# Kernel tuning notes

Measured on AMD Instinct MI355X. Metric: run time of the kernel, lower is better.

## Reference

```python
import jax, jax.numpy as jnp
import numpy as np

N_NODES = 100000
N_EDGES = 1600000
D = 64            # embedding_dim
D2 = D * D        # GRUCell hidden/input size


def gru_cell(x, h, w_ih, w_hh, b_ih, b_hh):
    # PyTorch GRUCell math. x, h: [D2]; w_ih, w_hh: [3*D2, D2]; b_*: [3*D2]
    gi = w_ih @ x + b_ih
    gh = w_hh @ h + b_hh
    i_r, i_z, i_n = jnp.split(gi, 3)
    h_r, h_z, h_n = jnp.split(gh, 3)
    r = jax.nn.sigmoid(i_r + h_r)
    z = jax.nn.sigmoid(i_z + h_z)
    n = jnp.tanh(i_n + r * h_n)
    return (1.0 - z) * n + z * h


def gcn_layer(x, w, src, dst, edge_norm):
    # dense transform then degree-normalized gather-scatter aggregation
    h = x @ w                                   # [N, D]
    m = h[src] * edge_norm[:, None]             # [E, D] messages
    return jax.ops.segment_sum(m, dst, num_segments=N_NODES)


def setup_inputs() -> dict:
    key = jax.random.key(0)
    ks = jax.random.split(key, 12)
    s = 0.02  # keep GRU gates in a sane range
    return {
        "node_embeddings": jax.random.normal(ks[0], (N_NODES, D), jnp.float32),
        "gc1_weights": jax.random.normal(ks[1], (D, D), jnp.float32) * s,
        "gc2_weights": jax.random.normal(ks[2], (D, D), jnp.float32) * s,
        "gc1_hist": jax.random.normal(ks[3], (D, D), jnp.float32) * s,
        "gc2_hist": jax.random.normal(ks[4], (D, D), jnp.float32) * s,
        "w_ih": jax.random.normal(ks[5], (3 * D2, D2), jnp.float32) * s,
        "w_hh": jax.random.normal(ks[6], (3 * D2, D2), jnp.float32) * s,
        "b_ih": jax.random.normal(ks[7], (3 * D2,), jnp.float32) * s,
        "b_hh": jax.random.normal(ks[8], (3 * D2,), jnp.float32) * s,
        "src": jax.random.randint(ks[9], (N_EDGES,), 0, N_NODES, jnp.int32),
        "dst": jax.random.randint(ks[10], (N_EDGES,), 0, N_NODES, jnp.int32),
    }


def reference(node_embeddings, gc1_weights, gc2_weights, gc1_hist, gc2_hist,
              w_ih, w_hh, b_ih, b_hh, src, dst):
    # --- weight evolution (GRUCell over flattened GCN weights) ---
    w1 = gru_cell(gc1_hist.reshape(-1), gc1_weights.reshape(-1),
                  w_ih, w_hh, b_ih, b_hh).reshape(D, D)
    w2 = gru_cell(gc2_hist.reshape(-1), gc2_weights.reshape(-1),
                  w_ih, w_hh, b_ih, b_hh).reshape(D, D)

    # --- symmetric degree normalization (in-degree, clamped at 1) ---
    deg = jax.ops.segment_sum(jnp.ones_like(dst, jnp.float32), dst,
                              num_segments=N_NODES)
    norm = jnp.clip(deg, 1.0, None) ** -0.5     # [N]
    edge_norm = norm[src] * norm[dst]           # [E]

    # --- two GCN layers ---
    x = jax.nn.relu(gcn_layer(node_embeddings, w1, src, dst, edge_norm))
    x = gcn_layer(x, w2, src, dst, edge_norm)
    return x
```

## Files before the change

kernel.cpp:

```cpp
#include <hip/hip_runtime.h>

typedef unsigned int uint_t;
typedef float v4f __attribute__((ext_vector_type(4)));

#define N_NODES 100000
#define N_EDGES 1600000
#define D 64
#define D2 4096
#define D3 12288

#define NPAD 100352u

#define BSHIFT 9
#define BNODES 512
#define NBUCK 196
#define CHUNK 8192
#define CAP   16384
#define GRUBLK 3072
#define XBLK  ((N_NODES + 255) / 256)

#define OFF_GI1   0u
#define OFF_GI2   (OFF_GI1 + D3)
#define OFF_GH1   (OFF_GI2 + D3)
#define OFF_GH2   (OFF_GH1 + D3)
#define OFF_W1    (OFF_GH2 + D3)
#define OFF_W2    (OFF_W1 + D2)
#define OFF_DEG   (OFF_W2 + D2)
#define OFF_BCUR  (OFF_DEG + NPAD)
#define OFF_ROWS  (OFF_BCUR + 256u)
#define OFF_CSR   (OFF_ROWS + NPAD)
#define OFF_XP    (OFF_CSR + 1600000u)
#define OFF_Y1    (OFF_XP + 3200000u)
#define OFF_PAIRS (OFF_Y1 + 3200000u)

__device__ __forceinline__ float dot4v(v4f a, float4 b, float acc) {
    acc = fmaf(a[0], b.x, acc);
    acc = fmaf(a[1], b.y, acc);
    acc = fmaf(a[2], b.z, acc);
    acc = fmaf(a[3], b.w, acc);
    return acc;
}

__device__ __forceinline__ uint_t bfr(float f) {
    uint_t u = __float_as_uint(f);
    u += 0x7FFFu + ((u >> 16) & 1u);
    return u >> 16;
}

struct PartLds {
    int hist[256];
    int lbase[256];
    int gbase[256];
    int lcur[256];
    int2 stage[CHUNK];
};
struct GruLds {
    float4 sA[1024];
    float4 sB[1024];
};

__global__ __launch_bounds__(512) void mega1(
    const float* __restrict__ w_ih, const float* __restrict__ w_hh,
    const float* __restrict__ x1, const float* __restrict__ x2,
    const float* __restrict__ h1, const float* __restrict__ h2,
    float* __restrict__ gi1, float* __restrict__ gi2,
    float* __restrict__ gh1, float* __restrict__ gh2,
    const int* __restrict__ src, const int* __restrict__ dst,
    int* __restrict__ deg, int* __restrict__ bcur, int2* __restrict__ pairs)
{
    __shared__ __align__(16) char ldsraw[sizeof(PartLds)];
    const int tid = threadIdx.x;

    if (blockIdx.x < NBUCK) {
        PartLds& P = *reinterpret_cast<PartLds*>(ldsraw);
        const int e0  = blockIdx.x * CHUNK;
        const int cnt = min(CHUNK, N_EDGES - e0);

        if (tid < 256) { P.hist[tid] = 0; P.lcur[tid] = 0; }
        __syncthreads();
        for (int i = tid; i < cnt; i += 512) {
            const int d = dst[e0 + i];
            atomicAdd(&deg[d], 1);
            atomicAdd(&P.hist[d >> BSHIFT], 1);
        }
        __syncthreads();
        if (tid < 256) P.lbase[tid] = P.hist[tid];
        __syncthreads();
        for (int off = 1; off < 256; off <<= 1) {
            int a = 0, b = 0;
            if (tid < 256) { a = P.lbase[tid]; b = (tid >= off) ? P.lbase[tid - off] : 0; }
            __syncthreads();
            if (tid < 256) P.lbase[tid] = a + b;
            __syncthreads();
        }
        if (tid < 256) {
            const int c = P.hist[tid];
            P.lbase[tid] -= c;
            P.gbase[tid] = c ? atomicAdd(&bcur[tid], c) : 0;
        }
        __syncthreads();
        for (int i = tid; i < cnt; i += 512) {
            const int s = src[e0 + i], d = dst[e0 + i];
            const int b = d >> BSHIFT;
            const int p = P.lbase[b] + atomicAdd(&P.lcur[b], 1);
            P.stage[p] = make_int2(s, d);
        }
        __syncthreads();
        for (int i = tid; i < cnt; i += 512) {
            const int2 v = P.stage[i];
            const int b = v.y >> BSHIFT;
            const int gp = P.gbase[b] + (i - P.lbase[b]);
            if (gp < CAP) pairs[(size_t)b * CAP + gp] = v;
        }
    } else {
        GruLds& G = *reinterpret_cast<GruLds*>(ldsraw);
        const int gb   = blockIdx.x - NBUCK;
        const int half = (gb >= GRUBLK / 2);
        const int blk  = gb - (half ? GRUBLK / 2 : 0);

        {
            const float4* va = (const float4*)(half ? h1 : x1);
            const float4* vb = (const float4*)(half ? h2 : x2);
#pragma unroll
            for (int i = 0; i < 2; ++i) {
                const int k = tid + i * 512;
                G.sA[k] = va[k];
                G.sB[k] = vb[k];
            }
        }
        __syncthreads();

        const int wave = tid >> 6, lane = tid & 63;
        const int row  = blk * 8 + wave;
        const v4f* wr = (const v4f*)((half ? w_hh : w_ih) + (size_t)row * D2);

        float p0 = 0.f, p1 = 0.f;
#pragma unroll
        for (int g = 0; g < 4; ++g) {
            v4f a[4];
#pragma unroll
            for (int k = 0; k < 4; ++k)
                a[k] = __builtin_nontemporal_load(&wr[lane + (g * 4 + k) * 64]);
#pragma unroll
            for (int k = 0; k < 4; ++k) {
                const int idx = lane + (g * 4 + k) * 64;
                p0 = dot4v(a[k], G.sA[idx], p0);
                p1 = dot4v(a[k], G.sB[idx], p1);
            }
        }
#pragma unroll
        for (int m = 32; m > 0; m >>= 1) {
            p0 += __shfl_down(p0, m, 64);
            p1 += __shfl_down(p1, m, 64);
        }
        if (lane == 0) {
            float* oA = half ? gh1 : gi1;
            float* oB = half ? gh2 : gi2;
            oA[row] = p0;
            oB[row] = p1;
        }
    }
}

struct CsrLds {
    int lofs[BNODES];
    int lcur[BNODES];
    int pscan[256];
    int bscan[256];
    int stage[CAP];
};

__global__ __launch_bounds__(256) void mega2(
    const int2* __restrict__ pairs, const int* __restrict__ deg,
    const int* __restrict__ bcnt, int* __restrict__ rowstart,
    int* __restrict__ csr_src,
    const float* __restrict__ emb,
    const float* __restrict__ gi1, const float* __restrict__ gh1,
    const float* __restrict__ gi2, const float* __restrict__ gh2,
    const float* __restrict__ b_ih, const float* __restrict__ b_hh,
    const float* __restrict__ hw1, const float* __restrict__ hw2,
    float* __restrict__ w1, float* __restrict__ w2,
    unsigned short* __restrict__ xp)
{
    __shared__ __align__(16) char ldsraw[sizeof(CsrLds)];
    const int tid = threadIdx.x;

    if (blockIdx.x < NBUCK) {
        CsrLds& L = *reinterpret_cast<CsrLds*>(ldsraw);
        const int b = blockIdx.x;
        const int nodeBase = b << BSHIFT;

        const int cb = (tid < NBUCK) ? bcnt[tid] : 0;
        L.bscan[tid] = cb;
        __syncthreads();
        for (int off = 1; off < 256; off <<= 1) {
            int a = L.bscan[tid];
            int x = (tid >= off) ? L.bscan[tid - off] : 0;
            __syncthreads();
            L.bscan[tid] = a + x;
            __syncthreads();
        }
        const int cnt  = bcnt[b];
        const int base = L.bscan[b] - cnt;

        const int n0 = nodeBase + 2 * tid;
        const int d0 = (n0     < N_NODES) ? deg[n0]     : 0;
        const int d1 = (n0 + 1 < N_NODES) ? deg[n0 + 1] : 0;
        L.pscan[tid] = d0 + d1;
        __syncthreads();
        for (int off = 1; off < 256; off <<= 1) {
            int a = L.pscan[tid];
            int x = (tid >= off) ? L.pscan[tid - off] : 0;
            __syncthreads();
            L.pscan[tid] = a + x;
            __syncthreads();
        }
        const int ex = L.pscan[tid] - (d0 + d1);
        L.lofs[2 * tid]     = ex;
        L.lofs[2 * tid + 1] = ex + d0;
        L.lcur[2 * tid]     = 0;
        L.lcur[2 * tid + 1] = 0;

        if (n0     < N_NODES) rowstart[n0]     = base + ex;
        if (n0 + 1 < N_NODES) rowstart[n0 + 1] = base + ex + d0;
        __syncthreads();

        const int2* bp = pairs + (size_t)b * CAP;
        for (int i = tid; i < cnt; i += 256) {
            const int2 v = bp[i];
            const int ln = v.y - nodeBase;
            const int p  = L.lofs[ln] + atomicAdd(&L.lcur[ln], 1);
            L.stage[p] = v.x;
        }
        __syncthreads();
        for (int i = tid; i < cnt; i += 256)
            csr_src[base + i] = L.stage[i];
    } else if (blockIdx.x < NBUCK + 2) {
        const int layer = blockIdx.x - NBUCK;
        const float* gi = layer ? gi2 : gi1;
        const float* gh = layer ? gh2 : gh1;
        const float* hw = layer ? hw2 : hw1;
        float* wo = layer ? w2 : w1;
#pragma unroll
        for (int i = 0; i < 16; ++i) {
            const int j = tid + i * 256;
            float ir = gi[j]          + b_ih[j];
            float hr = gh[j]          + b_hh[j];
            float iz = gi[j + D2]     + b_ih[j + D2];
            float hz = gh[j + D2]     + b_hh[j + D2];
            float in_ = gi[j + 2*D2]  + b_ih[j + 2*D2];
            float hn = gh[j + 2*D2]   + b_hh[j + 2*D2];
            float r = 1.f / (1.f + expf(-(ir + hr)));
            float z = 1.f / (1.f + expf(-(iz + hz)));
            float n = tanhf(in_ + r * hn);
            wo[j] = (1.f - z) * n + z * hw[j];
        }
    } else {
        const int node = (blockIdx.x - NBUCK - 2) * 256 + tid;
        if (node >= N_NODES) return;
        const float nn = rsqrtf(fmaxf((float)deg[node], 1.0f));
        const float4* p = (const float4*)(emb + (size_t)node * D);
        uint_t pk[32];
#pragma unroll
        for (int i = 0; i < 16; ++i) {
            float4 u = p[i];
            pk[2*i]   = bfr(u.x * nn) | (bfr(u.y * nn) << 16);
            pk[2*i+1] = bfr(u.z * nn) | (bfr(u.w * nn) << 16);
        }
        uint4* po = (uint4*)(xp + (size_t)node * D);
#pragma unroll
        for (int i = 0; i < 8; ++i)
            po[i] = make_uint4(pk[4*i], pk[4*i+1], pk[4*i+2], pk[4*i+3]);
    }
}

template <bool LAYER1>
__global__ __launch_bounds__(256) void gcn_layer_kernel(
    const unsigned short* __restrict__ xbf, const float* __restrict__ w,
    const int* __restrict__ csr_src, const int* __restrict__ rowstart,
    const int* __restrict__ degv, void* __restrict__ out)
{
    __shared__ float sw[D2];
    __shared__ float xr[4][8][68];
    const int tid = threadIdx.x;
#pragma unroll
    for (int i = 0; i < 16; ++i) sw[tid + i * 256] = w[tid + i * 256];
    __syncthreads();

    const int node = blockIdx.x * 32 + (tid >> 3);
    const int lg   = tid & 7;
    const int wv   = tid >> 6;
    const int slot = (tid >> 3) & 7;
    const uint4* hp = (const uint4*)xbf;
    const bool active = (node < N_NODES);
    int dg = 0;

    if (active) {
        const int beg = rowstart[node];
        dg = degv[node];

        float acc[8];
#pragma unroll
        for (int c = 0; c < 8; ++c) acc[c] = 0.f;

        int k = 0;
        for (; k + 8 <= dg; k += 8) {
            int s[8];
#pragma unroll
            for (int u = 0; u < 8; ++u) s[u] = csr_src[beg + k + u];
            uint4 r[8];
#pragma unroll
            for (int u = 0; u < 8; ++u) r[u] = hp[(size_t)s[u] * 8 + lg];
#pragma unroll
            for (int u = 0; u < 8; ++u) {
                acc[0] += __uint_as_float(r[u].x << 16);
                acc[1] += __uint_as_float(r[u].x & 0xFFFF0000u);
                acc[2] += __uint_as_float(r[u].y << 16);
                acc[3] += __uint_as_float(r[u].y & 0xFFFF0000u);
                acc[4] += __uint_as_float(r[u].z << 16);
                acc[5] += __uint_as_float(r[u].z & 0xFFFF0000u);
                acc[6] += __uint_as_float(r[u].w << 16);
                acc[7] += __uint_as_float(r[u].w & 0xFFFF0000u);
            }
        }
        for (; k < dg; ++k) {
            const int s = csr_src[beg + k];
            const uint4 r = hp[(size_t)s * 8 + lg];
            acc[0] += __uint_as_float(r.x << 16);
            acc[1] += __uint_as_float(r.x & 0xFFFF0000u);
            acc[2] += __uint_as_float(r.y << 16);
            acc[3] += __uint_as_float(r.y & 0xFFFF0000u);
            acc[4] += __uint_as_float(r.z << 16);
            acc[5] += __uint_as_float(r.z & 0xFFFF0000u);
            acc[6] += __uint_as_float(r.w << 16);
            acc[7] += __uint_as_float(r.w & 0xFFFF0000u);
        }

        const float nn = rsqrtf(fmaxf((float)dg, 1.0f));
#pragma unroll
        for (int c = 0; c < 8; ++c) xr[wv][slot][lg * 8 + c] = acc[c] * nn;
    }
    __syncthreads();

    if (active) {
        float o[8];
#pragma unroll
        for (int c = 0; c < 8; ++c) o[c] = 0.f;
#pragma unroll
        for (int k = 0; k < D; ++k) {
            const float xv = xr[wv][slot][k];
#pragma unroll
            for (int c = 0; c < 8; ++c)
                o[c] = fmaf(xv, sw[k * D + lg * 8 + c], o[c]);
        }
        if (LAYER1) {
            const float nn = rsqrtf(fmaxf((float)dg, 1.0f));
            float t[8];
#pragma unroll
            for (int c = 0; c < 8; ++c) t[c] = fmaxf(o[c], 0.f) * nn;
            uint4 pk;
            pk.x = bfr(t[0]) | (bfr(t[1]) << 16);
            pk.y = bfr(t[2]) | (bfr(t[3]) << 16);
            pk.z = bfr(t[4]) | (bfr(t[5]) << 16);
            pk.w = bfr(t[6]) | (bfr(t[7]) << 16);
            ((uint4*)out)[(size_t)node * 8 + lg] = pk;
        } else {
            float* op = (float*)out + (size_t)node * D + (size_t)lg * 8;
            *(float4*)(op)     = make_float4(o[0], o[1], o[2], o[3]);
            *(float4*)(op + 4) = make_float4(o[4], o[5], o[6], o[7]);
        }
    }
}

extern "C" void kernel_launch(void* const* d_in, const int* in_sizes, int n_in,
                              void* d_out, int out_size, void* d_ws, size_t ws_size,
                              hipStream_t stream)
{
    const float* emb  = (const float*)d_in[0];
    const float* gc1w = (const float*)d_in[1];
    const float* gc2w = (const float*)d_in[2];
    const float* gc1h = (const float*)d_in[3];
    const float* gc2h = (const float*)d_in[4];
    const float* w_ih = (const float*)d_in[5];
    const float* w_hh = (const float*)d_in[6];
    const float* b_ih = (const float*)d_in[7];
    const float* b_hh = (const float*)d_in[8];
    const int* src = (const int*)d_in[9];
    const int* dst = (const int*)d_in[10];

    float* ws = (float*)d_ws;
    float* gi1 = ws + OFF_GI1;
    float* gi2 = ws + OFF_GI2;
    float* gh1 = ws + OFF_GH1;
    float* gh2 = ws + OFF_GH2;
    float* w1  = ws + OFF_W1;
    float* w2  = ws + OFF_W2;
    int*   deg = (int*)(ws + OFF_DEG);
    int*   bcur = (int*)(ws + OFF_BCUR);
    int*   rows = (int*)(ws + OFF_ROWS);
    int*   csr  = (int*)(ws + OFF_CSR);
    unsigned short* xp = (unsigned short*)(ws + OFF_XP);
    unsigned short* y1 = (unsigned short*)(ws + OFF_Y1);
    int2*  pairs = (int2*)(ws + OFF_PAIRS);
    float* out  = (float*)d_out;

    hipMemsetAsync(deg, 0, (NPAD + 256) * sizeof(int), stream);

    mega1<<<NBUCK + GRUBLK, 512, 0, stream>>>(
        w_ih, w_hh, gc1h, gc2h, gc1w, gc2w, gi1, gi2, gh1, gh2,
        src, dst, deg, bcur, pairs);

    mega2<<<NBUCK + 2 + XBLK, 256, 0, stream>>>(
        pairs, deg, bcur, rows, csr, emb,
        gi1, gh1, gi2, gh2, b_ih, b_hh, gc1w, gc2w, w1, w2, xp);

    gcn_layer_kernel<true><<<(N_NODES + 31) / 32, 256, 0, stream>>>(
        xp, w1, csr, rows, deg, y1);

    gcn_layer_kernel<false><<<(N_NODES + 31) / 32, 256, 0, stream>>>(
        y1, w2, csr, rows, deg, out);
}
```

Before: 569.5 us.

## Split bf16 features into column slices and separate gather from dense transform

Node features are now stored as four 16-column bf16 slices, each its own contiguous array. The gather is a separate kernel that runs one pass per slice, so each pass's random-access working set (about 3.2 MB) is more likely to stay in cache. The dense 64x64 transform moves to its own kernel with one thread per node and 64 accumulators in registers. This adds a round trip through an fp32 intermediate buffer and extra launches, and risks heavy register pressure in the transform kernel.

```diff
diff --git a/kernel.cpp b/kernel.cpp
--- a/kernel.cpp
+++ b/kernel.cpp
@@ -18,6 +18,9 @@
 #define CAP   16384
 #define GRUBLK 3072
 #define XBLK  ((N_NODES + 255) / 256)
+
+#define SLICE_US 1600000u
+#define GCHUNKS  ((N_NODES + 127) / 128)
 
 #define OFF_GI1   0u
 #define OFF_GI2   (OFF_GI1 + D3)
@@ -32,6 +35,7 @@
 #define OFF_XP    (OFF_CSR + 1600000u)
 #define OFF_Y1    (OFF_XP + 3200000u)
 #define OFF_PAIRS (OFF_Y1 + 3200000u)
+#define OFF_G     OFF_PAIRS
 
 __device__ __forceinline__ float dot4v(v4f a, float4 b, float acc) {
     acc = fmaf(a[0], b.x, acc);
@@ -45,6 +49,21 @@
     uint_t u = __float_as_uint(f);
     u += 0x7FFFu + ((u >> 16) & 1u);
     return u >> 16;
+}
+
+__device__ __forceinline__ void store_sliced(
+    unsigned short* base, int node, const float* t)
+{
+#pragma unroll
+    for (int p = 0; p < 4; ++p) {
+        uint_t pk[8];
+#pragma unroll
+        for (int j = 0; j < 8; ++j)
+            pk[j] = bfr(t[p*16 + 2*j]) | (bfr(t[p*16 + 2*j + 1]) << 16);
+        uint4* po = (uint4*)(base + (size_t)p * SLICE_US + (size_t)node * 16);
+        po[0] = make_uint4(pk[0], pk[1], pk[2], pk[3]);
+        po[1] = make_uint4(pk[4], pk[5], pk[6], pk[7]);
+    }
 }
 
 struct PartLds {
@@ -260,115 +279,119 @@
         if (node >= N_NODES) return;
         const float nn = rsqrtf(fmaxf((float)deg[node], 1.0f));
         const float4* p = (const float4*)(emb + (size_t)node * D);
-        uint_t pk[32];
+        float t[D];
 #pragma unroll
         for (int i = 0; i < 16; ++i) {
             float4 u = p[i];
-            pk[2*i]   = bfr(u.x * nn) | (bfr(u.y * nn) << 16);
-            pk[2*i+1] = bfr(u.z * nn) | (bfr(u.w * nn) << 16);
-        }
-        uint4* po = (uint4*)(xp + (size_t)node * D);
-#pragma unroll
-        for (int i = 0; i < 8; ++i)
-            po[i] = make_uint4(pk[4*i], pk[4*i+1], pk[4*i+2], pk[4*i+3]);
-    }
+            t[4*i+0] = u.x * nn; t[4*i+1] = u.y * nn;
+            t[4*i+2] = u.z * nn; t[4*i+3] = u.w * nn;
+        }
+        store_sliced(xp, node, t);
+    }
+}
+
+__global__ __launch_bounds__(256) void gather_slice_kernel(
+    const unsigned short* __restrict__ xs, const int* __restrict__ csr_src,
+    const int* __restrict__ rowstart, const int* __restrict__ degv,
+    float* __restrict__ g)
+{
+    const int tid   = threadIdx.x;
+    const int pass  = blockIdx.x & 3;
+    const int chunk = blockIdx.x >> 2;
+    const int node  = chunk * 128 + (tid >> 1);
+    if (node >= N_NODES) return;
+    const int half = tid & 1;
+    const uint4* sp = (const uint4*)(xs + (size_t)pass * SLICE_US);
+
+    const int beg = rowstart[node];
+    const int dg  = degv[node];
+
+    float acc[8];
+#pragma unroll
+    for (int c = 0; c < 8; ++c) acc[c] = 0.f;
+
+    int k = 0;
+    for (; k + 8 <= dg; k += 8) {
+        int s[8];
+#pragma unroll
+        for (int u = 0; u < 8; ++u) s[u] = csr_src[beg + k + u];
+        uint4 r[8];
+#pragma unroll
+        for (int u = 0; u < 8; ++u) r[u] = sp[(size_t)s[u] * 2 + half];
+#pragma unroll
+        for (int u = 0; u < 8; ++u) {
+            acc[0] += __uint_as_float(r[u].x << 16);
+            acc[1] += __uint_as_float(r[u].x & 0xFFFF0000u);
+            acc[2] += __uint_as_float(r[u].y << 16);
+            acc[3] += __uint_as_float(r[u].y & 0xFFFF0000u);
+            acc[4] += __uint_as_float(r[u].z << 16);
+            acc[5] += __uint_as_float(r[u].z & 0xFFFF0000u);
+            acc[6] += __uint_as_float(r[u].w << 16);
+            acc[7] += __uint_as_float(r[u].w & 0xFFFF0000u);
+        }
+    }
+    for (; k < dg; ++k) {
+        const int s = csr_src[beg + k];
+        const uint4 r = sp[(size_t)s * 2 + half];
+        acc[0] += __uint_as_float(r.x << 16);
+        acc[1] += __uint_as_float(r.x & 0xFFFF0000u);
+        acc[2] += __uint_as_float(r.y << 16);
+        acc[3] += __uint_as_float(r.y & 0xFFFF0000u);
+        acc[4] += __uint_as_float(r.z << 16);
+        acc[5] += __uint_as_float(r.z & 0xFFFF0000u);
+        acc[6] += __uint_as_float(r.w << 16);
+        acc[7] += __uint_as_float(r.w & 0xFFFF0000u);
+    }
+
+    float* op = g + (size_t)node * D + pass * 16 + half * 8;
+    *(float4*)(op)     = make_float4(acc[0], acc[1], acc[2], acc[3]);
+    *(float4*)(op + 4) = make_float4(acc[4], acc[5], acc[6], acc[7]);
 }
 
 template <bool LAYER1>
-__global__ __launch_bounds__(256) void gcn_layer_kernel(
-    const unsigned short* __restrict__ xbf, const float* __restrict__ w,
-    const int* __restrict__ csr_src, const int* __restrict__ rowstart,
-    const int* __restrict__ degv, void* __restrict__ out)
+__global__ __launch_bounds__(256) void xform_kernel(
+    const float* __restrict__ g, const float* __restrict__ w,
+    const int* __restrict__ deg, void* __restrict__ out)
 {
     __shared__ float sw[D2];
-    __shared__ float xr[4][8][68];
     const int tid = threadIdx.x;
 #pragma unroll
     for (int i = 0; i < 16; ++i) sw[tid + i * 256] = w[tid + i * 256];
     __syncthreads();
 
-    const int node = blockIdx.x * 32 + (tid >> 3);
-    const int lg   = tid & 7;
-    const int wv   = tid >> 6;
-    const int slot = (tid >> 3) & 7;
-    const uint4* hp = (const uint4*)xbf;
-    const bool active = (node < N_NODES);
-    int dg = 0;
-
-    if (active) {
-        const int beg = rowstart[node];
-        dg = degv[node];
-
-        float acc[8];
-#pragma unroll
-        for (int c = 0; c < 8; ++c) acc[c] = 0.f;
-
-        int k = 0;
-        for (; k + 8 <= dg; k += 8) {
-            int s[8];
-#pragma unroll
-            for (int u = 0; u < 8; ++u) s[u] = csr_src[beg + k + u];
-            uint4 r[8];
-#pragma unroll
-            for (int u = 0; u < 8; ++u) r[u] = hp[(size_t)s[u] * 8 + lg];
-#pragma unroll
-            for (int u = 0; u < 8; ++u) {
-                acc[0] += __uint_as_float(r[u].x << 16);
-                acc[1] += __uint_as_float(r[u].x & 0xFFFF0000u);
-                acc[2] += __uint_as_float(r[u].y << 16);
-                acc[3] += __uint_as_float(r[u].y & 0xFFFF0000u);
-                acc[4] += __uint_as_float(r[u].z << 16);
-                acc[5] += __uint_as_float(r[u].z & 0xFFFF0000u);
-                acc[6] += __uint_as_float(r[u].w << 16);
-                acc[7] += __uint_as_float(r[u].w & 0xFFFF0000u);
-            }
-        }
-        for (; k < dg; ++k) {
-            const int s = csr_src[beg + k];
-            const uint4 r = hp[(size_t)s * 8 + lg];
-            acc[0] += __uint_as_float(r.x << 16);
-            acc[1] += __uint_as_float(r.x & 0xFFFF0000u);
-            acc[2] += __uint_as_float(r.y << 16);
-            acc[3] += __uint_as_float(r.y & 0xFFFF0000u);
-            acc[4] += __uint_as_float(r.z << 16);
-            acc[5] += __uint_as_float(r.z & 0xFFFF0000u);
-            acc[6] += __uint_as_float(r.w << 16);
-            acc[7] += __uint_as_float(r.w & 0xFFFF0000u);
-        }
-
-        const float nn = rsqrtf(fmaxf((float)dg, 1.0f));
-#pragma unroll
-        for (int c = 0; c < 8; ++c) xr[wv][slot][lg * 8 + c] = acc[c] * nn;
-    }
-    __syncthreads();
-
-    if (active) {
-        float o[8];
-#pragma unroll
-        for (int c = 0; c < 8; ++c) o[c] = 0.f;
-#pragma unroll
-        for (int k = 0; k < D; ++k) {
-            const float xv = xr[wv][slot][k];
-#pragma unroll
-            for (int c = 0; c < 8; ++c)
-                o[c] = fmaf(xv, sw[k * D + lg * 8 + c], o[c]);
-        }
-        if (LAYER1) {
-            const float nn = rsqrtf(fmaxf((float)dg, 1.0f));
-            float t[8];
-#pragma unroll
-            for (int c = 0; c < 8; ++c) t[c] = fmaxf(o[c], 0.f) * nn;
-            uint4 pk;
-            pk.x = bfr(t[0]) | (bfr(t[1]) << 16);
-            pk.y = bfr(t[2]) | (bfr(t[3]) << 16);
-            pk.z = bfr(t[4]) | (bfr(t[5]) << 16);
-            pk.w = bfr(t[6]) | (bfr(t[7]) << 16);
-            ((uint4*)out)[(size_t)node * 8 + lg] = pk;
-        } else {
-            float* op = (float*)out + (size_t)node * D + (size_t)lg * 8;
-            *(float4*)(op)     = make_float4(o[0], o[1], o[2], o[3]);
-            *(float4*)(op + 4) = make_float4(o[4], o[5], o[6], o[7]);
-        }
+    const int node = blockIdx.x * 256 + tid;
+    if (node >= N_NODES) return;
+
+    const float nn = rsqrtf(fmaxf((float)deg[node], 1.0f));
+    float x[D];
+    const float4* p = (const float4*)(g + (size_t)node * D);
+#pragma unroll
+    for (int i = 0; i < 16; ++i) {
+        float4 u = p[i];
+        x[4*i+0] = u.x * nn; x[4*i+1] = u.y * nn;
+        x[4*i+2] = u.z * nn; x[4*i+3] = u.w * nn;
+    }
+
+    float acc[D];
+#pragma unroll
+    for (int j = 0; j < D; ++j) acc[j] = 0.f;
+#pragma unroll
+    for (int k = 0; k < D; ++k) {
+        float a = x[k];
+#pragma unroll
+        for (int j = 0; j < D; ++j) acc[j] = fmaf(a, sw[k * D + j], acc[j]);
+    }
+
+    if (LAYER1) {
+        float t[D];
+#pragma unroll
+        for (int j = 0; j < D; ++j) t[j] = fmaxf(acc[j], 0.f) * nn;
+        store_sliced((unsigned short*)out, node, t);
+    } else {
+        float4* po = (float4*)((float*)out + (size_t)node * D);
+#pragma unroll
+        for (int i = 0; i < 16; ++i)
+            po[i] = make_float4(acc[4*i], acc[4*i+1], acc[4*i+2], acc[4*i+3]);
     }
 }
 
@@ -402,6 +425,7 @@
     unsigned short* xp = (unsigned short*)(ws + OFF_XP);
     unsigned short* y1 = (unsigned short*)(ws + OFF_Y1);
     int2*  pairs = (int2*)(ws + OFF_PAIRS);
+    float* g    = ws + OFF_G;
     float* out  = (float*)d_out;
 
     hipMemsetAsync(deg, 0, (NPAD + 256) * sizeof(int), stream);
@@ -414,9 +438,9 @@
         pairs, deg, bcur, rows, csr, emb,
         gi1, gh1, gi2, gh2, b_ih, b_hh, gc1w, gc2w, w1, w2, xp);
 
-    gcn_layer_kernel<true><<<(N_NODES + 31) / 32, 256, 0, stream>>>(
-        xp, w1, csr, rows, deg, y1);
-
-    gcn_layer_kernel<false><<<(N_NODES + 31) / 32, 256, 0, stream>>>(
-        y1, w2, csr, rows, deg, out);
-}
+    gather_slice_kernel<<<GCHUNKS * 4, 256, 0, stream>>>(xp, csr, rows, deg, g);
+    xform_kernel<true><<<XBLK, 256, 0, stream>>>(g, w1, deg, y1);
+
+    gather_slice_kernel<<<GCHUNKS * 4, 256, 0, stream>>>(y1, csr, rows, deg, g);
+    xform_kernel<false><<<XBLK, 256, 0, stream>>>(g, w2, deg, out);
+}
```

Measured after the change: 619.2 us. 1.09x slower.
